# Optimization experiments

Hardware: AMD Instinct MI355X
Metric: run time of the kernel (lower is better)

## Reference

```python
import jax, jax.numpy as jnp
import numpy as np

N_NODES = 50000
N_EDGES = 800000
NUM_FEATURES = 256
HIDDEN = 256
HEADS = 8
OUT_DIM = 2


def setup_inputs() -> dict:
    key = jax.random.key(0)
    ks = jax.random.split(key, 16)
    C1 = HIDDEN // HEADS  # 32 per-head channels
    inp = {
        'x': jax.random.normal(ks[0], (N_NODES, NUM_FEATURES), dtype=jnp.float32),
        'edge_index': jax.random.randint(ks[1], (2, N_EDGES), 0, N_NODES, dtype=jnp.int64),
        # layer 1: num_features -> heads * (hidden//heads)
        'W1': jax.random.normal(ks[2], (NUM_FEATURES, HEADS * C1), dtype=jnp.float32) * 0.05,
        'att_src1': jax.random.normal(ks[3], (HEADS, C1), dtype=jnp.float32) * 0.1,
        'att_dst1': jax.random.normal(ks[4], (HEADS, C1), dtype=jnp.float32) * 0.1,
        'b1': jnp.zeros((HEADS * C1,), dtype=jnp.float32),
        # layer 2: hidden -> heads * (hidden//heads)
        'W2': jax.random.normal(ks[5], (HIDDEN, HEADS * C1), dtype=jnp.float32) * 0.05,
        'att_src2': jax.random.normal(ks[6], (HEADS, C1), dtype=jnp.float32) * 0.1,
        'att_dst2': jax.random.normal(ks[7], (HEADS, C1), dtype=jnp.float32) * 0.1,
        'b2': jnp.zeros((HEADS * C1,), dtype=jnp.float32),
        # layer 3: hidden -> output_dim, heads=1, concat=False
        'W3': jax.random.normal(ks[8], (HIDDEN, OUT_DIM), dtype=jnp.float32) * 0.05,
        'att_src3': jax.random.normal(ks[9], (1, OUT_DIM), dtype=jnp.float32) * 0.1,
        'att_dst3': jax.random.normal(ks[10], (1, OUT_DIM), dtype=jnp.float32) * 0.1,
        'b3': jnp.zeros((OUT_DIM,), dtype=jnp.float32),
    }
    return inp


def _gat_layer(x, src, dst, W, a_src, a_dst, b, concat):
    # PyG GATConv: h = x W -> [N, H, C]; e_ij = leaky_relu(a_src.h_j + a_dst.h_i)
    # softmax over edges grouped by destination, then scatter-add h_j * alpha.
    N = x.shape[0]
    H, C = a_src.shape
    h = (x @ W).reshape(N, H, C)
    alpha_s = jnp.einsum('nhc,hc->nh', h, a_src)  # [N, H]
    alpha_d = jnp.einsum('nhc,hc->nh', h, a_dst)
    e = jax.nn.leaky_relu(alpha_s[src] + alpha_d[dst], negative_slope=0.2)  # [E, H]
    m = jax.ops.segment_max(e, dst, num_segments=N)  # per-dst max for stable softmax
    ee = jnp.exp(e - m[dst])
    denom = jax.ops.segment_sum(ee, dst, num_segments=N)
    alpha = ee / (denom[dst] + 1e-16)  # [E, H]
    msg = h[src] * alpha[:, :, None]  # [E, H, C]
    out = jax.ops.segment_sum(msg, dst, num_segments=N)  # [N, H, C]
    out = out.reshape(N, H * C) if concat else out.mean(axis=1)
    return out + b


def reference(x, edge_index, W1, att_src1, att_dst1, b1, W2, att_src2, att_dst2, b2, W3, att_src3, att_dst3, b3):
    N = x.shape[0]
    loops = jnp.arange(N, dtype=edge_index.dtype)
    src = jnp.concatenate([edge_index[0], loops])  # PyG add_self_loops=True
    dst = jnp.concatenate([edge_index[1], loops])
    h = _gat_layer(x, src, dst, W1, att_src1, att_dst1, b1, concat=True)
    h = jax.nn.elu(h)  # dropout is identity in eval mode
    h = _gat_layer(h, src, dst, W2, att_src2, att_dst2, b2, concat=True)
    h = jax.nn.elu(h)
    out = _gat_layer(h, src, dst, W3, att_src3, att_dst3, b3, concat=False)
    return out  # [N, output_dim]; batch=None so pooling/MLP head is skipped
```

## Files before the change

### kernel.cpp

```cpp
#include <hip/hip_runtime.h>
#include <math.h>

#define NF 256
#define NHEADS 8
#define MNEG -1e30f

typedef _Float16 half8 __attribute__((ext_vector_type(8)));
typedef _Float16 half4 __attribute__((ext_vector_type(4)));
typedef float f32x4 __attribute__((ext_vector_type(4)));


__global__ __launch_bounds__(256) void deg_count_k(const int* __restrict__ dst, int* __restrict__ deg, int E) {
    int e = blockIdx.x * 256 + threadIdx.x;
    if (e < E) atomicAdd(&deg[dst[e]], 1);
}

__global__ __launch_bounds__(256) void scan1_k(const int* __restrict__ deg, int* __restrict__ indptr,
                                               int* __restrict__ bsum, int n) {
    __shared__ int sh[256];
    int tid = threadIdx.x;
    int i = blockIdx.x * 256 + tid;
    int d = (i < n) ? deg[i] : 0;
    sh[tid] = d;
    __syncthreads();
#pragma unroll
    for (int off = 1; off < 256; off <<= 1) {
        int t = (tid >= off) ? sh[tid - off] : 0;
        __syncthreads();
        sh[tid] += t;
        __syncthreads();
    }
    if (i < n) indptr[i] = sh[tid] - d;
    if (tid == 255) bsum[blockIdx.x] = sh[255];
}

__global__ __launch_bounds__(256) void scan2_k(int* __restrict__ bsum, int* __restrict__ boff, int nb) {
    __shared__ int sh[256];
    int tid = threadIdx.x;
    int d = (tid < nb) ? bsum[tid] : 0;
    sh[tid] = d;
    __syncthreads();
#pragma unroll
    for (int off = 1; off < 256; off <<= 1) {
        int t = (tid >= off) ? sh[tid - off] : 0;
        __syncthreads();
        sh[tid] += t;
        __syncthreads();
    }
    if (tid < nb) boff[tid] = sh[tid] - d;
}

__global__ __launch_bounds__(256) void scan3_k(const int* __restrict__ deg, int* __restrict__ indptr,
                                               const int* __restrict__ boff, int* __restrict__ cursor,
                                               int* __restrict__ srcs, int n) {
    int i = blockIdx.x * 256 + threadIdx.x;
    if (i < n) {
        int v = indptr[i] + boff[blockIdx.x] + i;
        indptr[i] = v;
        srcs[v] = i;
        cursor[i] = v + 1;
        if (i == n - 1) indptr[n] = v + deg[i] + 1;
    }
}

__global__ __launch_bounds__(256) void fill_edge_k(const int* __restrict__ esrc, const int* __restrict__ edst,
                                                   int* __restrict__ cursor, int* __restrict__ srcs, int E) {
    int e = blockIdx.x * 256 + threadIdx.x;
    if (e < E) {
        int p = atomicAdd(&cursor[edst[e]], 1);
        srcs[p] = esrc[e];
    }
}


__global__ __launch_bounds__(256) void prep_w_k(const float* __restrict__ W, _Float16* __restrict__ WTh) {
    int tid = blockIdx.x * 256 + threadIdx.x;
    int k = tid >> 8, c = tid & 255;
    WTh[(size_t)c * 256 + k] = (_Float16)W[(size_t)k * 256 + c];
}


template <int AF32>
__global__ __launch_bounds__(512, 2) void gemm_mfma_k(const void* __restrict__ Av, const _Float16* __restrict__ WTh,
                                                      const float* __restrict__ att_s, const float* __restrict__ att_d,
                                                      _Float16* __restrict__ C, float* __restrict__ aS,
                                                      float* __restrict__ aD, int M) {
    __shared__ __align__(16) _Float16 WT[256][264];
    int t = threadIdx.x;
#pragma unroll
    for (int it = 0; it < 16; ++it) {
        int col = it * 16 + (t >> 5);
        int kc = (t & 31) * 8;
        *(half8*)&WT[col][kc] = *(const half8*)&WTh[(size_t)col * 256 + kc];
    }
    __syncthreads();

    int wave = t >> 6, lane = t & 63;
    int wm = wave >> 2, wn = wave & 3;
    int lr = lane & 15, lg = lane >> 4;
    int r0 = blockIdx.x * 256 + wm * 128;
    int c0 = wn * 64;
    const float* Af = (const float*)Av;
    const _Float16* Ah = (const _Float16*)Av;

    f32x4 acc[8][4];
#pragma unroll
    for (int mr = 0; mr < 8; ++mr)
#pragma unroll
        for (int nr = 0; nr < 4; ++nr) acc[mr][nr] = (f32x4){0.f, 0.f, 0.f, 0.f};

    for (int ks = 0; ks < 8; ++ks) {
        int k0 = ks * 32;
        half8 a[8];
#pragma unroll
        for (int mr = 0; mr < 8; ++mr) {
            int row = r0 + mr * 16 + lr;
            row = row < M ? row : M - 1;
            if (AF32) {
                const float* p = Af + (size_t)row * 256 + k0 + lg * 8;
                float4 x0 = *(const float4*)p;
                float4 x1 = *(const float4*)(p + 4);
                half8 av;
                av[0] = (_Float16)x0.x; av[1] = (_Float16)x0.y; av[2] = (_Float16)x0.z; av[3] = (_Float16)x0.w;
                av[4] = (_Float16)x1.x; av[5] = (_Float16)x1.y; av[6] = (_Float16)x1.z; av[7] = (_Float16)x1.w;
                a[mr] = av;
            } else {
                a[mr] = *(const half8*)(Ah + (size_t)row * 256 + k0 + lg * 8);
            }
        }
        half8 b[4];
#pragma unroll
        for (int nr = 0; nr < 4; ++nr)
            b[nr] = *(const half8*)&WT[c0 + nr * 16 + lr][k0 + lg * 8];
#pragma unroll
        for (int mr = 0; mr < 8; ++mr)
#pragma unroll
            for (int nr = 0; nr < 4; ++nr)
                acc[mr][nr] = __builtin_amdgcn_mfma_f32_16x16x32_f16(a[mr], b[nr], acc[mr][nr], 0, 0, 0);
    }

    int h0 = wn * 2, h1 = wn * 2 + 1;
    float as_c0 = att_s[h0 * 32 + lr],      as_c1 = att_s[h0 * 32 + 16 + lr];
    float as_c2 = att_s[h1 * 32 + lr],      as_c3 = att_s[h1 * 32 + 16 + lr];
    float ad_c0 = att_d[h0 * 32 + lr],      ad_c1 = att_d[h0 * 32 + 16 + lr];
    float ad_c2 = att_d[h1 * 32 + lr],      ad_c3 = att_d[h1 * 32 + 16 + lr];

#pragma unroll
    for (int mr = 0; mr < 8; ++mr) {
        int rbase = r0 + mr * 16 + lg * 4;
#pragma unroll
        for (int j = 0; j < 4; ++j) {
            int row = rbase + j;
            float ps0 = acc[mr][0][j] * as_c0 + acc[mr][1][j] * as_c1;
            float ps1 = acc[mr][2][j] * as_c2 + acc[mr][3][j] * as_c3;
            float pd0 = acc[mr][0][j] * ad_c0 + acc[mr][1][j] * ad_c1;
            float pd1 = acc[mr][2][j] * ad_c2 + acc[mr][3][j] * ad_c3;
#pragma unroll
            for (int o = 1; o < 16; o <<= 1) {
                ps0 += __shfl_xor(ps0, o);
                ps1 += __shfl_xor(ps1, o);
                pd0 += __shfl_xor(pd0, o);
                pd1 += __shfl_xor(pd1, o);
            }
            if (row < M) {
#pragma unroll
                for (int nr = 0; nr < 4; ++nr)
                    C[(size_t)row * 256 + c0 + nr * 16 + lr] = (_Float16)acc[mr][nr][j];
                if (lr == 0) {
                    aS[(size_t)row * NHEADS + h0] = ps0;
                    aS[(size_t)row * NHEADS + h1] = ps1;
                    aD[(size_t)row * NHEADS + h0] = pd0;
                    aD[(size_t)row * NHEADS + h1] = pd1;
                }
            }
        }
    }
}


template <int MODE>
__global__ __launch_bounds__(256) void agg_k(const _Float16* __restrict__ h, const float* __restrict__ aS,
                                             const float* __restrict__ aD, const int* __restrict__ indptr,
                                             const int* __restrict__ srcs, const float* __restrict__ bias,
                                             _Float16* __restrict__ out,
                                             const float* __restrict__ W3, const float* __restrict__ as3,
                                             const float* __restrict__ ad3, float* __restrict__ h3,
                                             float* __restrict__ s3, float* __restrict__ d3, int N) {
    int wid = blockIdx.x * 4 + (threadIdx.x >> 6);
    if (wid >= N) return;
    int lane = threadIdx.x & 63;
    int hf = lane >> 5;
    int cl = lane & 31;
    int hh = cl >> 2;
    float ad = aD[(size_t)wid * NHEADS + hh];
    int beg = indptr[wid], end = indptr[wid + 1];
    const half8* h8p = (const half8*)h;
    float m = MNEG, den = 0.f;
    float a0 = 0, a1 = 0, a2 = 0, a3 = 0, a4 = 0, a5 = 0, a6 = 0, a7 = 0;
    int k = beg;
    for (; k + 8 <= end; k += 8) {
        int s[4]; float as[4]; half8 v[4]; float e[4], p[4];
#pragma unroll
        for (int j = 0; j < 4; ++j) s[j] = srcs[k + 2 * j + hf];
#pragma unroll
        for (int j = 0; j < 4; ++j) as[j] = aS[(size_t)s[j] * NHEADS + hh];
#pragma unroll
        for (int j = 0; j < 4; ++j) v[j] = h8p[(size_t)s[j] * 32 + cl];
#pragma unroll
        for (int j = 0; j < 4; ++j) { e[j] = as[j] + ad; e[j] = (e[j] > 0.f) ? e[j] : 0.2f * e[j]; }
        float em = fmaxf(fmaxf(e[0], e[1]), fmaxf(e[2], e[3]));
        if (__any(em > m + 8.f)) {
            float mn = fmaxf(m, em);
            float sc = __expf(m - mn);
            den *= sc; a0 *= sc; a1 *= sc; a2 *= sc; a3 *= sc; a4 *= sc; a5 *= sc; a6 *= sc; a7 *= sc;
            m = mn;
        }
#pragma unroll
        for (int j = 0; j < 4; ++j) p[j] = __expf(e[j] - m);
#pragma unroll
        for (int j = 0; j < 4; ++j) {
            den += p[j];
            a0 += p[j] * (float)v[j][0]; a1 += p[j] * (float)v[j][1];
            a2 += p[j] * (float)v[j][2]; a3 += p[j] * (float)v[j][3];
            a4 += p[j] * (float)v[j][4]; a5 += p[j] * (float)v[j][5];
            a6 += p[j] * (float)v[j][6]; a7 += p[j] * (float)v[j][7];
        }
    }
    for (; k + 2 <= end; k += 2) {
        int s = srcs[k + hf];
        float as = aS[(size_t)s * NHEADS + hh];
        half8 v = h8p[(size_t)s * 32 + cl];
        float e = as + ad; e = (e > 0.f) ? e : 0.2f * e;
        if (__any(e > m + 8.f)) {
            float mn = fmaxf(m, e);
            float sc = __expf(m - mn);
            den *= sc; a0 *= sc; a1 *= sc; a2 *= sc; a3 *= sc; a4 *= sc; a5 *= sc; a6 *= sc; a7 *= sc;
            m = mn;
        }
        float p = __expf(e - m);
        den += p;
        a0 += p * (float)v[0]; a1 += p * (float)v[1]; a2 += p * (float)v[2]; a3 += p * (float)v[3];
        a4 += p * (float)v[4]; a5 += p * (float)v[5]; a6 += p * (float)v[6]; a7 += p * (float)v[7];
    }
    if (k < end) {
        int s = srcs[k];
        float e = aS[(size_t)s * NHEADS + hh] + ad;
        e = (e > 0.f) ? e : 0.2f * e;
        half8 v = h8p[(size_t)s * 32 + cl];
        float eg = (hf == 0) ? e : MNEG;
        if (__any(eg > m + 8.f)) {
            float mn = fmaxf(m, eg);
            float sc = __expf(m - mn);
            den *= sc; a0 *= sc; a1 *= sc; a2 *= sc; a3 *= sc; a4 *= sc; a5 *= sc; a6 *= sc; a7 *= sc;
            m = mn;
        }
        float p = (hf == 0) ? __expf(e - m) : 0.f;
        den += p;
        a0 += p * (float)v[0]; a1 += p * (float)v[1]; a2 += p * (float)v[2]; a3 += p * (float)v[3];
        a4 += p * (float)v[4]; a5 += p * (float)v[5]; a6 += p * (float)v[6]; a7 += p * (float)v[7];
    }
    {
        float m2 = __shfl_xor(m, 32);
        float den2 = __shfl_xor(den, 32);
        float mn = fmaxf(m, m2);
        float sc1 = __expf(m - mn), sc2 = __expf(m2 - mn);
        den = den * sc1 + den2 * sc2;
        a0 = a0 * sc1 + __shfl_xor(a0, 32) * sc2;
        a1 = a1 * sc1 + __shfl_xor(a1, 32) * sc2;
        a2 = a2 * sc1 + __shfl_xor(a2, 32) * sc2;
        a3 = a3 * sc1 + __shfl_xor(a3, 32) * sc2;
        a4 = a4 * sc1 + __shfl_xor(a4, 32) * sc2;
        a5 = a5 * sc1 + __shfl_xor(a5, 32) * sc2;
        a6 = a6 * sc1 + __shfl_xor(a6, 32) * sc2;
        a7 = a7 * sc1 + __shfl_xor(a7, 32) * sc2;
    }
    float inv = 1.f / (den + 1e-16f);
    float4 bv0 = *(const float4*)&bias[cl * 8];
    float4 bv1 = *(const float4*)&bias[cl * 8 + 4];
    float o[8];
    o[0] = a0 * inv + bv0.x; o[1] = a1 * inv + bv0.y; o[2] = a2 * inv + bv0.z; o[3] = a3 * inv + bv0.w;
    o[4] = a4 * inv + bv1.x; o[5] = a5 * inv + bv1.y; o[6] = a6 * inv + bv1.z; o[7] = a7 * inv + bv1.w;
#pragma unroll
    for (int c = 0; c < 8; ++c) o[c] = (o[c] > 0.f) ? o[c] : expm1f(o[c]);

    if (MODE == 0) {
        if (hf == 0) {
            half8 ov;
#pragma unroll
            for (int c = 0; c < 8; ++c) ov[c] = (_Float16)o[c];
            ((half8*)out)[(size_t)wid * 32 + cl] = ov;
        }
    } else {
        const float4* W34 = (const float4*)W3;
        float p0 = 0.f, p1 = 0.f;
#pragma unroll
        for (int q = 0; q < 4; ++q) {
            float4 w = W34[cl * 4 + q];
            p0 += o[2 * q] * w.x + o[2 * q + 1] * w.z;
            p1 += o[2 * q] * w.y + o[2 * q + 1] * w.w;
        }
#pragma unroll
        for (int off = 1; off < 32; off <<= 1) {
            p0 += __shfl_xor(p0, off);
            p1 += __shfl_xor(p1, off);
        }
        if (lane == 0) {
            h3[(size_t)wid * 2] = p0;
            h3[(size_t)wid * 2 + 1] = p1;
            s3[wid] = p0 * as3[0] + p1 * as3[1];
            d3[wid] = p0 * ad3[0] + p1 * ad3[1];
        }
    }
}


__global__ __launch_bounds__(256) void agg3_k(const float* __restrict__ h3, const float* __restrict__ s3,
                                              const float* __restrict__ d3, const int* __restrict__ indptr,
                                              const int* __restrict__ srcs, const float* __restrict__ b3,
                                              float* __restrict__ out, int N) {
    int t = blockIdx.x * 256 + threadIdx.x;
    int n = t >> 2;
    if (n >= N) return;
    int sub = t & 3;
    float ad = d3[n];
    float m = MNEG, den = 0.f, a0 = 0.f, a1 = 0.f;
    int beg = indptr[n], end = indptr[n + 1];
    for (int k = beg + sub; k < end; k += 4) {
        int s = srcs[k];
        float e = s3[s] + ad;
        e = (e > 0.f) ? e : 0.2f * e;
        if (e > m + 8.f) {
            float mn = fmaxf(m, e);
            float sc = __expf(m - mn);
            den *= sc; a0 *= sc; a1 *= sc;
            m = mn;
        }
        float p = __expf(e - m);
        den += p;
        a0 += p * h3[(size_t)s * 2];
        a1 += p * h3[(size_t)s * 2 + 1];
    }
#pragma unroll
    for (int off = 1; off < 4; off <<= 1) {
        float m2 = __shfl_xor(m, off);
        float den2 = __shfl_xor(den, off);
        float a02 = __shfl_xor(a0, off);
        float a12 = __shfl_xor(a1, off);
        float mn = fmaxf(m, m2);
        float sc1 = __expf(m - mn);
        float sc2 = __expf(m2 - mn);
        den = den * sc1 + den2 * sc2;
        a0 = a0 * sc1 + a02 * sc2;
        a1 = a1 * sc1 + a12 * sc2;
        m = mn;
    }
    if (sub == 0) {
        float inv = 1.f / (den + 1e-16f);
        out[(size_t)n * 2]     = a0 * inv + b3[0];
        out[(size_t)n * 2 + 1] = a1 * inv + b3[1];
    }
}


extern "C" void kernel_launch(void* const* d_in, const int* in_sizes, int n_in,
                              void* d_out, int out_size, void* d_ws, size_t ws_size,
                              hipStream_t stream) {
    const float* x   = (const float*)d_in[0];
    const int*   ei  = (const int*)d_in[1];
    const float* W1  = (const float*)d_in[2];
    const float* as1 = (const float*)d_in[3];
    const float* ad1 = (const float*)d_in[4];
    const float* b1  = (const float*)d_in[5];
    const float* W2  = (const float*)d_in[6];
    const float* as2 = (const float*)d_in[7];
    const float* ad2 = (const float*)d_in[8];
    const float* b2  = (const float*)d_in[9];
    const float* W3  = (const float*)d_in[10];
    const float* at_s3 = (const float*)d_in[11];
    const float* at_d3 = (const float*)d_in[12];
    const float* b3  = (const float*)d_in[13];

    int N = in_sizes[0] / NF;
    int E = in_sizes[1] / 2;
    const int* esrc = ei;
    const int* edst = ei + E;

    char* w = (char*)d_ws;
    _Float16* hbuf  = (_Float16*)w; w += (size_t)N * NF * 2;
    _Float16* xnext = (_Float16*)w; w += (size_t)N * NF * 2;
    float* aS    = (float*)w; w += (size_t)N * NHEADS * 4;
    float* aD    = (float*)w; w += (size_t)N * NHEADS * 4;
    float* h3    = (float*)w; w += (size_t)N * 2 * 4;
    float* s3    = (float*)w; w += (size_t)N * 4;
    float* d3    = (float*)w; w += (size_t)N * 4;
    int* deg     = (int*)w; w += (size_t)N * 4;
    int* indptr  = (int*)w; w += (size_t)(N + 1) * 4 + 60;
    int* cursor  = (int*)w; w += (size_t)N * 4;
    int* bsum    = (int*)w; w += 256 * 4;
    int* boff    = (int*)w; w += 256 * 4;
    _Float16* WTh1 = (_Float16*)w; w += (size_t)256 * 256 * 2;
    _Float16* WTh2 = (_Float16*)w; w += (size_t)256 * 256 * 2;
    int* srcs    = (int*)w;

    int nb_n = (N + 255) / 256;
    int nb_e = (E + 255) / 256;
    int nb_w = (N + 3) / 4;
    int nb_g = (N + 255) / 256;
    int nb_a3 = (N * 4 + 255) / 256;

    hipMemsetAsync(deg, 0, (size_t)N * 4, stream);
    deg_count_k<<<nb_e, 256, 0, stream>>>(edst, deg, E);
    scan1_k<<<nb_n, 256, 0, stream>>>(deg, indptr, bsum, N);
    scan2_k<<<1, 256, 0, stream>>>(bsum, boff, nb_n);
    scan3_k<<<nb_n, 256, 0, stream>>>(deg, indptr, boff, cursor, srcs, N);
    fill_edge_k<<<nb_e, 256, 0, stream>>>(esrc, edst, cursor, srcs, E);
    prep_w_k<<<256, 256, 0, stream>>>(W1, WTh1);
    prep_w_k<<<256, 256, 0, stream>>>(W2, WTh2);

    gemm_mfma_k<1><<<nb_g, 512, 0, stream>>>(x, WTh1, as1, ad1, hbuf, aS, aD, N);
    agg_k<0><<<nb_w, 256, 0, stream>>>(hbuf, aS, aD, indptr, srcs, b1, xnext,
                                       nullptr, nullptr, nullptr, nullptr, nullptr, nullptr, N);
    gemm_mfma_k<0><<<nb_g, 512, 0, stream>>>(xnext, WTh2, as2, ad2, hbuf, aS, aD, N);
    agg_k<1><<<nb_w, 256, 0, stream>>>(hbuf, aS, aD, indptr, srcs, b2, nullptr,
                                       W3, at_s3, at_d3, h3, s3, d3, N);
    agg3_k<<<nb_a3, 256, 0, stream>>>(h3, s3, d3, indptr, srcs, b3, (float*)d_out, N);
}
```

Baseline: 326.9 us.

## Fuse scan passes and weight prep, prefetch srcs, use fp16 packed accumulation in aggregation

Merges the block-offset scan into the final scan kernel, with each block recomputing the prefix of block sums, and merges the two weight-transpose launches into one. Together these remove two kernel launches. The aggregation loop now prefetches the next batch of source indices, uses fmaxf for leaky ReLU, and lowers the rescale threshold. Each 4-edge batch is accumulated as packed fp16 multiply-adds before being added to the fp32 accumulators. The fp16 partial sums cost some precision in exchange for fewer float conversions and FMAs.

```diff
diff --git a/kernel.cpp b/kernel.cpp
--- a/kernel.cpp
+++ b/kernel.cpp
@@ -6,7 +6,6 @@
 #define MNEG -1e30f
 
 typedef _Float16 half8 __attribute__((ext_vector_type(8)));
-typedef _Float16 half4 __attribute__((ext_vector_type(4)));
 typedef float f32x4 __attribute__((ext_vector_type(4)));
 
 
@@ -34,7 +33,9 @@
     if (tid == 255) bsum[blockIdx.x] = sh[255];
 }
 
-__global__ __launch_bounds__(256) void scan2_k(int* __restrict__ bsum, int* __restrict__ boff, int nb) {
+__global__ __launch_bounds__(256) void scan3_k(const int* __restrict__ deg, int* __restrict__ indptr,
+                                               const int* __restrict__ bsum, int* __restrict__ cursor,
+                                               int* __restrict__ srcs, int n, int nb) {
     __shared__ int sh[256];
     int tid = threadIdx.x;
     int d = (tid < nb) ? bsum[tid] : 0;
@@ -47,15 +48,11 @@
         sh[tid] += t;
         __syncthreads();
     }
-    if (tid < nb) boff[tid] = sh[tid] - d;
-}
-
-__global__ __launch_bounds__(256) void scan3_k(const int* __restrict__ deg, int* __restrict__ indptr,
-                                               const int* __restrict__ boff, int* __restrict__ cursor,
-                                               int* __restrict__ srcs, int n) {
-    int i = blockIdx.x * 256 + threadIdx.x;
+    int bid = blockIdx.x;
+    int boff = sh[bid] - ((bid < nb) ? bsum[bid] : 0);
+    int i = bid * 256 + tid;
     if (i < n) {
-        int v = indptr[i] + boff[blockIdx.x] + i;
+        int v = indptr[i] + boff + i;
         indptr[i] = v;
         srcs[v] = i;
         cursor[i] = v + 1;
@@ -73,10 +70,14 @@
 }
 
 
-__global__ __launch_bounds__(256) void prep_w_k(const float* __restrict__ W, _Float16* __restrict__ WTh) {
+__global__ __launch_bounds__(256) void prep_w_k(const float* __restrict__ W1, const float* __restrict__ W2,
+                                                _Float16* __restrict__ O1, _Float16* __restrict__ O2) {
     int tid = blockIdx.x * 256 + threadIdx.x;
-    int k = tid >> 8, c = tid & 255;
-    WTh[(size_t)c * 256 + k] = (_Float16)W[(size_t)k * 256 + c];
+    const float* W = (tid < 65536) ? W1 : W2;
+    _Float16* O = (tid < 65536) ? O1 : O2;
+    int t = tid & 65535;
+    int k = t >> 8, c = t & 255;
+    O[(size_t)c * 256 + k] = (_Float16)W[t];
 }
 
 
@@ -196,68 +197,78 @@
     int beg = indptr[wid], end = indptr[wid + 1];
     const half8* h8p = (const half8*)h;
     float m = MNEG, den = 0.f;
-    float a0 = 0, a1 = 0, a2 = 0, a3 = 0, a4 = 0, a5 = 0, a6 = 0, a7 = 0;
+    float f0 = 0, f1 = 0, f2 = 0, f3 = 0, f4 = 0, f5 = 0, f6 = 0, f7 = 0;
     int k = beg;
+    int sp[4];
+    if (k + 8 <= end) {
+#pragma unroll
+        for (int j = 0; j < 4; ++j) sp[j] = srcs[k + 2 * j + hf];
+    }
     for (; k + 8 <= end; k += 8) {
-        int s[4]; float as[4]; half8 v[4]; float e[4], p[4];
-#pragma unroll
-        for (int j = 0; j < 4; ++j) s[j] = srcs[k + 2 * j + hf];
+        int s[4]; float as[4]; half8 v[4]; float e[4];
+#pragma unroll
+        for (int j = 0; j < 4; ++j) s[j] = sp[j];
+        if (k + 16 <= end) {
+#pragma unroll
+            for (int j = 0; j < 4; ++j) sp[j] = srcs[k + 8 + 2 * j + hf];
+        }
 #pragma unroll
         for (int j = 0; j < 4; ++j) as[j] = aS[(size_t)s[j] * NHEADS + hh];
 #pragma unroll
         for (int j = 0; j < 4; ++j) v[j] = h8p[(size_t)s[j] * 32 + cl];
 #pragma unroll
-        for (int j = 0; j < 4; ++j) { e[j] = as[j] + ad; e[j] = (e[j] > 0.f) ? e[j] : 0.2f * e[j]; }
+        for (int j = 0; j < 4; ++j) { e[j] = as[j] + ad; e[j] = fmaxf(e[j], 0.2f * e[j]); }
         float em = fmaxf(fmaxf(e[0], e[1]), fmaxf(e[2], e[3]));
-        if (__any(em > m + 8.f)) {
+        if (__any(em > m + 4.f)) {
             float mn = fmaxf(m, em);
             float sc = __expf(m - mn);
-            den *= sc; a0 *= sc; a1 *= sc; a2 *= sc; a3 *= sc; a4 *= sc; a5 *= sc; a6 *= sc; a7 *= sc;
+            den *= sc; f0 *= sc; f1 *= sc; f2 *= sc; f3 *= sc; f4 *= sc; f5 *= sc; f6 *= sc; f7 *= sc;
             m = mn;
         }
-#pragma unroll
-        for (int j = 0; j < 4; ++j) p[j] = __expf(e[j] - m);
+        half8 hacc = (half8)(_Float16)0.f;
 #pragma unroll
         for (int j = 0; j < 4; ++j) {
-            den += p[j];
-            a0 += p[j] * (float)v[j][0]; a1 += p[j] * (float)v[j][1];
-            a2 += p[j] * (float)v[j][2]; a3 += p[j] * (float)v[j][3];
-            a4 += p[j] * (float)v[j][4]; a5 += p[j] * (float)v[j][5];
-            a6 += p[j] * (float)v[j][6]; a7 += p[j] * (float)v[j][7];
-        }
+            float p = __expf(e[j] - m);
+            den += p;
+            _Float16 ph = (_Float16)p;
+            half8 pb = {ph, ph, ph, ph, ph, ph, ph, ph};
+            hacc += v[j] * pb;
+        }
+        f0 += (float)hacc[0]; f1 += (float)hacc[1]; f2 += (float)hacc[2]; f3 += (float)hacc[3];
+        f4 += (float)hacc[4]; f5 += (float)hacc[5]; f6 += (float)hacc[6]; f7 += (float)hacc[7];
     }
     for (; k + 2 <= end; k += 2) {
         int s = srcs[k + hf];
         float as = aS[(size_t)s * NHEADS + hh];
         half8 v = h8p[(size_t)s * 32 + cl];
-        float e = as + ad; e = (e > 0.f) ? e : 0.2f * e;
-        if (__any(e > m + 8.f)) {
+        float e = as + ad; e = fmaxf(e, 0.2f * e);
+        if (__any(e > m + 4.f)) {
             float mn = fmaxf(m, e);
             float sc = __expf(m - mn);
-            den *= sc; a0 *= sc; a1 *= sc; a2 *= sc; a3 *= sc; a4 *= sc; a5 *= sc; a6 *= sc; a7 *= sc;
+            den *= sc; f0 *= sc; f1 *= sc; f2 *= sc; f3 *= sc; f4 *= sc; f5 *= sc; f6 *= sc; f7 *= sc;
             m = mn;
         }
         float p = __expf(e - m);
         den += p;
-        a0 += p * (float)v[0]; a1 += p * (float)v[1]; a2 += p * (float)v[2]; a3 += p * (float)v[3];
-        a4 += p * (float)v[4]; a5 += p * (float)v[5]; a6 += p * (float)v[6]; a7 += p * (float)v[7];
+        f0 += p * (float)v[0]; f1 += p * (float)v[1]; f2 += p * (float)v[2]; f3 += p * (float)v[3];
+        f4 += p * (float)v[4]; f5 += p * (float)v[5]; f6 += p * (float)v[6]; f7 += p * (float)v[7];
     }
     if (k < end) {
         int s = srcs[k];
         float e = aS[(size_t)s * NHEADS + hh] + ad;
-        e = (e > 0.f) ? e : 0.2f * e;
+        e = fmaxf(e, 0.2f * e);
         half8 v = h8p[(size_t)s * 32 + cl];
         float eg = (hf == 0) ? e : MNEG;
-        if (__any(eg > m + 8.f)) {
+        if (__any(eg > m + 4.f)) {
             float mn = fmaxf(m, eg);
             float sc = __expf(m - mn);
-            den *= sc; a0 *= sc; a1 *= sc; a2 *= sc; a3 *= sc; a4 *= sc; a5 *= sc; a6 *= sc; a7 *= sc;
+            den *= sc; f0 *= sc; f1 *= sc; f2 *= sc; f3 *= sc; f4 *= sc; f5 *= sc; f6 *= sc; f7 *= sc;
             m = mn;
         }
         float p = (hf == 0) ? __expf(e - m) : 0.f;
         den += p;
-        a0 += p * (float)v[0]; a1 += p * (float)v[1]; a2 += p * (float)v[2]; a3 += p * (float)v[3];
-        a4 += p * (float)v[4]; a5 += p * (float)v[5]; a6 += p * (float)v[6]; a7 += p * (float)v[7];
+        f0 += p * (float)v[0]; f1 += p * (float)v[1]; f2 += p * (float)v[2]; f3 += p * (float)v[3];
+        f4 += p * (float)v[4]; f5 += p * (float)v[5]; f6 += p * (float)v[6]; f7 += p * (float)v[7];
     }
     {
         float m2 = __shfl_xor(m, 32);
@@ -265,21 +276,21 @@
         float mn = fmaxf(m, m2);
         float sc1 = __expf(m - mn), sc2 = __expf(m2 - mn);
         den = den * sc1 + den2 * sc2;
-        a0 = a0 * sc1 + __shfl_xor(a0, 32) * sc2;
-        a1 = a1 * sc1 + __shfl_xor(a1, 32) * sc2;
-        a2 = a2 * sc1 + __shfl_xor(a2, 32) * sc2;
-        a3 = a3 * sc1 + __shfl_xor(a3, 32) * sc2;
-        a4 = a4 * sc1 + __shfl_xor(a4, 32) * sc2;
-        a5 = a5 * sc1 + __shfl_xor(a5, 32) * sc2;
-        a6 = a6 * sc1 + __shfl_xor(a6, 32) * sc2;
-        a7 = a7 * sc1 + __shfl_xor(a7, 32) * sc2;
+        f0 = f0 * sc1 + __shfl_xor(f0, 32) * sc2;
+        f1 = f1 * sc1 + __shfl_xor(f1, 32) * sc2;
+        f2 = f2 * sc1 + __shfl_xor(f2, 32) * sc2;
+        f3 = f3 * sc1 + __shfl_xor(f3, 32) * sc2;
+        f4 = f4 * sc1 + __shfl_xor(f4, 32) * sc2;
+        f5 = f5 * sc1 + __shfl_xor(f5, 32) * sc2;
+        f6 = f6 * sc1 + __shfl_xor(f6, 32) * sc2;
+        f7 = f7 * sc1 + __shfl_xor(f7, 32) * sc2;
     }
     float inv = 1.f / (den + 1e-16f);
     float4 bv0 = *(const float4*)&bias[cl * 8];
     float4 bv1 = *(const float4*)&bias[cl * 8 + 4];
     float o[8];
-    o[0] = a0 * inv + bv0.x; o[1] = a1 * inv + bv0.y; o[2] = a2 * inv + bv0.z; o[3] = a3 * inv + bv0.w;
-    o[4] = a4 * inv + bv1.x; o[5] = a5 * inv + bv1.y; o[6] = a6 * inv + bv1.z; o[7] = a7 * inv + bv1.w;
+    o[0] = f0 * inv + bv0.x; o[1] = f1 * inv + bv0.y; o[2] = f2 * inv + bv0.z; o[3] = f3 * inv + bv0.w;
+    o[4] = f4 * inv + bv1.x; o[5] = f5 * inv + bv1.y; o[6] = f6 * inv + bv1.z; o[7] = f7 * inv + bv1.w;
 #pragma unroll
     for (int c = 0; c < 8; ++c) o[c] = (o[c] > 0.f) ? o[c] : expm1f(o[c]);
 
@@ -328,7 +339,7 @@
     for (int k = beg + sub; k < end; k += 4) {
         int s = srcs[k];
         float e = s3[s] + ad;
-        e = (e > 0.f) ? e : 0.2f * e;
+        e = fmaxf(e, 0.2f * e);
         if (e > m + 8.f) {
             float mn = fmaxf(m, e);
             float sc = __expf(m - mn);
@@ -397,7 +408,6 @@
     int* indptr  = (int*)w; w += (size_t)(N + 1) * 4 + 60;
     int* cursor  = (int*)w; w += (size_t)N * 4;
     int* bsum    = (int*)w; w += 256 * 4;
-    int* boff    = (int*)w; w += 256 * 4;
     _Float16* WTh1 = (_Float16*)w; w += (size_t)256 * 256 * 2;
     _Float16* WTh2 = (_Float16*)w; w += (size_t)256 * 256 * 2;
     int* srcs    = (int*)w;
@@ -411,11 +421,9 @@
     hipMemsetAsync(deg, 0, (size_t)N * 4, stream);
     deg_count_k<<<nb_e, 256, 0, stream>>>(edst, deg, E);
     scan1_k<<<nb_n, 256, 0, stream>>>(deg, indptr, bsum, N);
-    scan2_k<<<1, 256, 0, stream>>>(bsum, boff, nb_n);
-    scan3_k<<<nb_n, 256, 0, stream>>>(deg, indptr, boff, cursor, srcs, N);
+    scan3_k<<<nb_n, 256, 0, stream>>>(deg, indptr, bsum, cursor, srcs, N, nb_n);
     fill_edge_k<<<nb_e, 256, 0, stream>>>(esrc, edst, cursor, srcs, E);
-    prep_w_k<<<256, 256, 0, stream>>>(W1, WTh1);
-    prep_w_k<<<256, 256, 0, stream>>>(W2, WTh2);
+    prep_w_k<<<512, 256, 0, stream>>>(W1, W2, WTh1, WTh2);
 
     gemm_mfma_k<1><<<nb_g, 512, 0, stream>>>(x, WTh1, as1, ad1, hbuf, aS, aD, N);
     agg_k<0><<<nb_w, 256, 0, stream>>>(hbuf, aS, aD, indptr, srcs, b1, xnext,
```

Measured after the change: 328.5 us. About the same (+0.5%).
